# Optimization experiments

Hardware: AMD Instinct MI355X
Metric: run time of the kernel (lower is better)

Reference implementation:

```python
import jax, jax.numpy as jnp
import numpy as np

B, N = 16, 512
CFL = 0.5


def _conv(x, k):
    return jax.lax.conv_general_dilated(x, k, (1, 1), 'VALID', dimension_numbers=('NHWC', 'HWIO', 'NHWC'))


def _pad(x, p):  # p = (top, bottom, left, right) spatial pads
    return jnp.pad(x, ((0, 0), (p[0], p[1]), (p[2], p[3]), (0, 0)))


def _t(k):  # transpose(perm=[1,0,2,3]) on an HWIO kernel
    return jnp.transpose(k, (1, 0, 2, 3))


def _amper(E, Hx, Hy, beta, delta, fb, fd, fy, kf, kb, fu, fdn):
    n = N
    s1 = (_pad(beta * _conv(Hy, _t(fb)) + delta * _conv(Hy, _t(fd)) + _conv(Hy, _t(fy)), (2, 2, 2, 2))
          + _pad(_conv(Hy, _t(kf)), (2, 2, 0, n - 1))
          + _pad(_conv(Hy, _t(kb)), (2, 2, n - 1, 0))
          + _pad(_conv(Hy, _t(fu)), (2, 2, 1, n - 2))
          + _pad(_conv(Hy, _t(fdn)), (2, 2, n - 2, 1)))
    s2 = (_pad(beta * _conv(Hx, fb) + delta * _conv(Hx, fd) + _conv(Hx, fy), (2, 2, 2, 2))
          + _pad(_conv(Hx, kf), (0, n - 1, 2, 2))
          + _pad(_conv(Hx, kb), (n - 1, 0, 2, 2))
          + _pad(_conv(Hx, fu), (1, n - 2, 2, 2))
          + _pad(_conv(Hx, fdn), (n - 2, 1, 2, 2)))
    return E + CFL * (s1 - s2)


def _faraday(E, Hx, Hy, beta, delta, fb, fd, fy, kef, keb):
    n = N
    s3 = (_pad(beta * _conv(E, fb) + delta * _conv(E, fd) + _conv(E, fy), (0, 0, 1, 1))
          + _pad(_conv(E, kef), (1, 1, 0, n - 2))[:, 1:-1, :, :]
          + _pad(_conv(E, keb), (1, 1, n - 2, 0))[:, 1:-1, :, :])
    s4 = (_pad(beta * _conv(E, _t(fb)) + delta * _conv(E, _t(fd)) + _conv(E, _t(fy)), (1, 1, 0, 0))
          + _pad(_conv(E, _t(kef)), (0, n - 2, 1, 1))[:, :, 1:-1, :]
          + _pad(_conv(E, _t(keb)), (n - 2, 0, 1, 1))[:, :, 1:-1, :])
    return Hx - CFL * s3, Hy + CFL * s4


def _forward(E1, Hx1, Hy1, beta, delta, fb, fd, fy, kf, kb, fu, fdn, kef, keb):
    E2 = _amper(E1, Hx1, Hy1, beta, delta, fb, fd, fy, kf, kb, fu, fdn)
    Hx2, Hy2 = _faraday(E2, Hx1, Hy1, beta, delta, fb, fd, fy, kef, keb)
    E3 = _amper(E2, Hx2, Hy2, beta, delta, fb, fd, fy, kf, kb, fu, fdn)
    Hx3, Hy3 = _faraday(E3, Hx2, Hy2, beta, delta, fb, fd, fy, kef, keb)
    E4 = _amper(E3, Hx3, Hy3, beta, delta, fb, fd, fy, kf, kb, fu, fdn)
    Hx4, Hy4 = _faraday(E4, Hx3, Hy3, beta, delta, fb, fd, fy, kef, keb)
    return (E2, Hx2, Hy2, E3, Hx3, Hy3, E4, Hx4, Hy4)


def setup_inputs():
    key = jax.random.key(0)
    ks = jax.random.split(key, 16)
    f32 = jnp.float32
    E_shape, Hx_shape, Hy_shape = (B, N + 1, N + 1, 1), (B, N - 1, N, 1), (B, N, N - 1, 1)
    # interior 2D DRP stencils (3x4): 4-tap staggered derivative x 3-tap transverse weights
    fy = np.zeros((3, 4, 1, 1), np.float32)
    fy[1, 1, 0, 0] = -1.0
    fy[1, 2, 0, 0] = 1.0
    fb = (np.outer([1.0, -2.0, 1.0], [0.0, -1.0, 1.0, 0.0]) / 8.0).astype(np.float32).reshape(3, 4, 1, 1)
    fd = (np.outer([0.0, 1.0, 0.0], [1.0, -3.0, 3.0, -1.0]) / 24.0).astype(np.float32).reshape(3, 4, 1, 1)
    rnd = lambda k, s: 0.05 * jax.random.normal(k, s, dtype=f32)
    return {
        'E1': jax.random.normal(ks[0], E_shape, f32),
        'Hx1': jax.random.normal(ks[1], Hx_shape, f32),
        'Hy1': jax.random.normal(ks[2], Hy_shape, f32),
        'E2': jax.random.normal(ks[3], E_shape, f32),
        'Hx2': jax.random.normal(ks[4], Hx_shape, f32),
        'Hy2': jax.random.normal(ks[5], Hy_shape, f32),
        'E3': jax.random.normal(ks[6], E_shape, f32),
        'Hx3': jax.random.normal(ks[7], Hx_shape, f32),
        'Hy3': jax.random.normal(ks[8], Hy_shape, f32),
        'beta': jnp.zeros((), f32),
        'delta': jnp.asarray([0.37], f32),
        'filter_beta': jnp.asarray(fb),
        'filter_delta': jnp.asarray(fd),
        'filter_yee': jnp.asarray(fy),
        'kernel_forward': rnd(ks[9], (N - 2, 4, 1, 1)),
        'kernel_backward': rnd(ks[10], (N - 2, 4, 1, 1)),
        'fourth_up': rnd(ks[11], (N - 2, 4, 1, 1)),
        'fourth_down': rnd(ks[12], (N - 2, 4, 1, 1)),
        'kernel_e_forward': rnd(ks[13], (3, N, 1, 1)),
        'kernel_e_backward': rnd(ks[14], (3, N, 1, 1)),
    }


def reference(E1, Hx1, Hy1, E2, Hx2, Hy2, E3, Hx3, Hy3, beta, delta, filter_beta, filter_delta, filter_yee, kernel_forward, kernel_backward, fourth_up, fourth_down, kernel_e_forward, kernel_e_backward):
    # Note: the original layer unpacks E2..Hy3 but never uses them.
    return _forward(E1, Hx1, Hy1, beta, delta, filter_beta, filter_delta, filter_yee,
                    kernel_forward, kernel_backward, fourth_up, fourth_down,
                    kernel_e_forward, kernel_e_backward)
```

## Files before the change

### kernel.cpp

```cpp
#include <hip/hip_runtime.h>

#define NB 16
#define NN 512
#define NP 513
#define NM 511
#define CFLc 0.5f

#define SE (NP*NP)
#define SHX (NM*NN)
#define SHY (NN*NM)

#define NCH 8
#define OFF_A 0
#define SZ_A (NB*NCH*6*512)
#define OFF_F (OFF_A + SZ_A)
#define SZ_F (NB*NCH*4*512)
#define OFF_SE (OFF_F + SZ_F)
#define SZ_SE (NB*6*NP)
#define OFF_SH (OFF_SE + SZ_SE)
#define SZ_SH (NB*4*NM)

__device__ __forceinline__ float dot4(float4 a, float4 b) {
    return a.x*b.x + a.y*b.y + a.z*b.z + a.w*b.w;
}

__device__ __forceinline__ void ld5(const float* __restrict__ a, int mb, float4* cr) {
    const float4* a4 = (const float4*)a;
    #pragma unroll
    for (int t = 0; t < 5; t++) {
        int idx = mb - 1 + t;
        if (idx >= 0 && idx <= 509) cr[t] = a4[idx];
        else cr[t] = make_float4(0.f, 0.f, 0.f, 0.f);
    }
}

__global__ __launch_bounds__(512, 4) void k_step1(
    const float* __restrict__ E, const float* __restrict__ Hx, const float* __restrict__ Hy,
    const float* __restrict__ beta, const float* __restrict__ delta,
    const float* __restrict__ fb, const float* __restrict__ fd, const float* __restrict__ fy,
    const float* __restrict__ kf, const float* __restrict__ kb,
    const float* __restrict__ fu, const float* __restrict__ fdn,
    float* __restrict__ ws, float* __restrict__ Eout,
    float* __restrict__ Hyfix, int fix)
{
    __shared__ float s_hy[7][512];
    __shared__ float s_hx[6][512];
    __shared__ float s_strip[8][6];
    __shared__ float gsm[12];

    int bid = blockIdx.x;
    int tid = threadIdx.x;

    if (bid < 128) {
        int b = bid >> 3;
        int chunk = bid & 7;
        int j = tid;
        if (j > 508) return;
        int p0 = chunk * 64;
        int p1 = min(510, p0 + 64);
        const float* Hxb = Hx + (size_t)b*SHX;
        float akf0=0,akf1=0,akb0=0,akb1=0,afu0=0,afu1=0,afd0=0,afd1=0;
        float r0v[4], r1v[4];
        #pragma unroll
        for (int q = 0; q < 4; q++) r0v[q] = Hxb[(size_t)p0*NN + j + q];
        for (int p = p0; p < p1; p++) {
            #pragma unroll
            for (int q = 0; q < 4; q++) r1v[q] = Hxb[(size_t)(p+1)*NN + j + q];
            #pragma unroll
            for (int q = 0; q < 4; q++) {
                float ckf = kf[p*4+q], ckb = kb[p*4+q], cfu = fu[p*4+q], cfd = fdn[p*4+q];
                akf0 += r0v[q]*ckf; akf1 += r1v[q]*ckf;
                akb0 += r0v[q]*ckb; akb1 += r1v[q]*ckb;
                afu0 += r0v[q]*cfu; afu1 += r1v[q]*cfu;
                afd0 += r0v[q]*cfd; afd1 += r1v[q]*cfd;
            }
            #pragma unroll
            for (int q = 0; q < 4; q++) r0v[q] = r1v[q];
        }
        float* o = ws + OFF_A + (((size_t)b*NCH + chunk)*6)*512 + j;
        o[0*512] = akf0;
        o[1*512] = akf1 + afu0;
        o[2*512] = afu1;
        o[3*512] = afd0;
        o[4*512] = afd1 + akb0;
        o[5*512] = akb1;
        return;
    }

    if (bid >= 2192) {
        if (!fix) return;
        int b = bid - 2192;
        int c = tid;
        if (c > 510) return;
        #pragma unroll
        for (int slot = 0; slot < 4; slot++) {
            int r = (slot < 2) ? slot : 508 + slot;
            float s = 0.f;
            #pragma unroll
            for (int ch = 0; ch < NCH; ch++)
                s += ws[OFF_F + (((size_t)b*NCH + ch)*4 + slot)*512 + c];
            Hyfix[(size_t)b*SHY + (size_t)r*NM + c] =
                ws[OFF_SH + ((size_t)b*4 + slot)*NM + c] + CFLc*s;
        }
        return;
    }

    int wrk = bid - 128;
    wrk = (wrk & 7) * 258 + (wrk >> 3);
    int rg = wrk >> 4;
    int b  = wrk & 15;
    int r0 = rg * 4;

    const float* Eb  = E  + (size_t)b*SE;
    const float* Hxb = Hx + (size_t)b*SHX;
    const float* Hyb = Hy + (size_t)b*SHY;
    int c = tid;

    if (tid < 12) gsm[tid] = beta[0]*fb[tid] + delta[0]*fd[tid] + fy[tid];
    #pragma unroll
    for (int k = 0; k < 7; k++) {
        int rm = min(max(r0-2+k, 0), 511);
        int cc = min(c, 510);
        float v;
        if (fix && (rm <= 1 || rm >= 510)) {
            int slot = (rm <= 1) ? rm : rm - 508;
            float s = 0.f;
            #pragma unroll
            for (int ch = 0; ch < NCH; ch++)
                s += ws[OFF_F + (((size_t)b*NCH + ch)*4 + slot)*512 + cc];
            v = ws[OFF_SH + ((size_t)b*4 + slot)*NM + cc] + CFLc*s;
        } else {
            v = Hyb[(size_t)rm*NM + cc];
        }
        s_hy[k][c] = v;
    }
    #pragma unroll
    for (int k = 0; k < 6; k++) {
        int rm = min(max(r0-2+k, 0), 510);
        s_hx[k][c] = Hxb[(size_t)rm*NN + c];
    }
    __syncthreads();

    {
        int w = tid >> 6, lane = tid & 63;
        int jj = w >> 1;
        int ii = r0 + jj - 2;
        if (ii >= 0 && ii <= 508) {
            int h = w & 1;
            int mb = h*256 + lane*4;
            float4 hv0 = *(const float4*)&s_hy[jj+0][mb];
            float4 hv1 = *(const float4*)&s_hy[jj+1][mb];
            float4 hv2 = *(const float4*)&s_hy[jj+2][mb];
            float4 hv3 = *(const float4*)&s_hy[jj+3][mb];
            float4 hc0 = make_float4(hv0.x, hv1.x, hv2.x, hv3.x);
            float4 hc1 = make_float4(hv0.y, hv1.y, hv2.y, hv3.y);
            float4 hc2 = make_float4(hv0.z, hv1.z, hv2.z, hv3.z);
            float4 hc3 = make_float4(hv0.w, hv1.w, hv2.w, hv3.w);
            float4 cr[5];
            ld5(kf, mb, cr);
            float pkf0 = dot4(hc0,cr[1]) + dot4(hc1,cr[2]) + dot4(hc2,cr[3]) + dot4(hc3,cr[4]);
            float pkf1 = dot4(hc0,cr[0]) + dot4(hc1,cr[1]) + dot4(hc2,cr[2]) + dot4(hc3,cr[3]);
            ld5(fu, mb, cr);
            float pfu0 = dot4(hc0,cr[1]) + dot4(hc1,cr[2]) + dot4(hc2,cr[3]) + dot4(hc3,cr[4]);
            float pfu1 = dot4(hc0,cr[0]) + dot4(hc1,cr[1]) + dot4(hc2,cr[2]) + dot4(hc3,cr[3]);
            ld5(fdn, mb, cr);
            float pfd0 = dot4(hc0,cr[1]) + dot4(hc1,cr[2]) + dot4(hc2,cr[3]) + dot4(hc3,cr[4]);
            float pfd1 = dot4(hc0,cr[0]) + dot4(hc1,cr[1]) + dot4(hc2,cr[2]) + dot4(hc3,cr[3]);
            ld5(kb, mb, cr);
            float pkb0 = dot4(hc0,cr[1]) + dot4(hc1,cr[2]) + dot4(hc2,cr[3]) + dot4(hc3,cr[4]);
            float pkb1 = dot4(hc0,cr[0]) + dot4(hc1,cr[1]) + dot4(hc2,cr[2]) + dot4(hc3,cr[3]);
            float v0 = pkf0;
            float v1 = pkf1 + pfu0;
            float v2 = pfu1;
            float v3 = pfd0;
            float v4 = pfd1 + pkb0;
            float v5 = pkb1;
            #pragma unroll
            for (int off = 32; off > 0; off >>= 1) {
                v0 += __shfl_down(v0, off);
                v1 += __shfl_down(v1, off);
                v2 += __shfl_down(v2, off);
                v3 += __shfl_down(v3, off);
                v4 += __shfl_down(v4, off);
                v5 += __shfl_down(v5, off);
            }
            if (lane == 0) {
                s_strip[w][0]=v0; s_strip[w][1]=v1; s_strip[w][2]=v2;
                s_strip[w][3]=v3; s_strip[w][4]=v4; s_strip[w][5]=v5;
            }
        }
    }
    __syncthreads();

    float g[12];
    #pragma unroll
    for (int i = 0; i < 12; i++) g[i] = gsm[i];

    int cy0 = min(max(c-2,0),510), cy1 = min(max(c-1,0),510), cy2 = min(c,510);
    int cx0 = max(c-2,0), cx1 = max(c-1,0), cx3 = min(c+1,511);
    float hyv[7][3];
    #pragma unroll
    for (int k = 0; k < 7; k++) {
        hyv[k][0]=s_hy[k][cy0]; hyv[k][1]=s_hy[k][cy1]; hyv[k][2]=s_hy[k][cy2];
    }
    float hxv[6][4];
    #pragma unroll
    for (int k = 0; k < 6; k++) {
        hxv[k][0]=s_hx[k][cx0]; hxv[k][1]=s_hx[k][cx1]; hxv[k][2]=s_hx[k][c]; hxv[k][3]=s_hx[k][cx3];
    }

    bool cint = (c >= 2 && c <= 510);
    int cslot = (c==0)?0:(c==1)?1:(c==2)?2:(c==510)?3:(c==511)?4:-1;
    float* Eo = Eout + (size_t)b*SE;

    #pragma unroll
    for (int j2 = 0; j2 < 4; j2++) {
        int r = r0 + j2;
        if (r > 512) break;
        float v = Eb[(size_t)r*NP + c];
        bool rint = (r >= 2 && r <= 510);
        if (rint && cint) {
            float s1 = 0.f, s2 = 0.f;
            #pragma unroll
            for (int p = 0; p < 4; p++)
                s1 += g[p]*hyv[j2+p][0] + g[4+p]*hyv[j2+p][1] + g[8+p]*hyv[j2+p][2];
            #pragma unroll
            for (int p = 0; p < 3; p++)
                s2 += g[p*4+0]*hxv[j2+p][0] + g[p*4+1]*hxv[j2+p][1]
                    + g[p*4+2]*hxv[j2+p][2] + g[p*4+3]*hxv[j2+p][3];
            v += CFLc * (s1 - s2);
        }
        if (rint && cslot >= 0)
            v += CFLc * (s_strip[2*j2][cslot] + s_strip[2*j2+1][cslot]);
        Eo[(size_t)r*NP + c] = v;
        bool rstrip = (r <= 2 || r >= 510);
        int rslot = (r <= 2) ? r : r - 507;
        if (rstrip)
            ws[OFF_SE + ((size_t)b*6 + rslot)*NP + c] = v;
        if (c == 511) {
            float v2 = Eb[(size_t)r*NP + 512];
            if (rint) v2 += CFLc * (s_strip[2*j2][5] + s_strip[2*j2+1][5]);
            Eo[(size_t)r*NP + 512] = v2;
            if (rstrip)
                ws[OFF_SE + ((size_t)b*6 + rslot)*NP + 512] = v2;
        }
    }
}

__global__ __launch_bounds__(512, 4) void k_step2(
    const float* __restrict__ E, const float* __restrict__ Hx, const float* __restrict__ Hy,
    const float* __restrict__ beta, const float* __restrict__ delta,
    const float* __restrict__ fb, const float* __restrict__ fd, const float* __restrict__ fy,
    const float* __restrict__ kef, const float* __restrict__ keb,
    float* __restrict__ ws, float* __restrict__ Hxout, float* __restrict__ Hyout,
    float* __restrict__ Efix)
{
    __shared__ float s_e[7][520];
    __shared__ float s_fix[3][NP];
    __shared__ float s_strip2[8][4];
    __shared__ float gsm[12];

    int bid = blockIdx.x;
    int tid = threadIdx.x;

    if (bid < 128) {
        int b = bid >> 3, chunk = bid & 7;
        const float* Eb = E + (size_t)b*SE;
        bool bnd = (chunk == 0 || chunk == 7);
        int rbase = (chunk == 0) ? 0 : 510;
        if (bnd) {
            int sbase = (chunk == 0) ? 0 : 3;
            for (int t = tid; t < 3*NP; t += 512) {
                int sr = t / NP, cc = t - sr*NP;
                int slot = sbase + sr;
                float v = ws[OFF_SE + ((size_t)b*6 + slot)*NP + cc];
                if (cc >= 2 && cc <= 510) {
                    float s = 0.f;
                    #pragma unroll
                    for (int ch = 0; ch < NCH; ch++)
                        s += ws[OFF_A + (((size_t)b*NCH + ch)*6 + slot)*512 + (cc-2)];
                    v -= CFLc * s;
                }
                s_fix[sr][cc] = v;
            }
            __syncthreads();
        }
        int c = tid;
        if (c > 510) return;
        int p0 = chunk*64, p1 = p0 + 64;
        auto ldE = [&](int rr, int col) -> float {
            if (bnd) {
                unsigned d = (unsigned)(rr - rbase);
                if (d < 3u) return s_fix[d][col];
            }
            return Eb[(size_t)rr*NP + col];
        };
        float af0=0, af1=0, ab0=0, ab1=0;
        float r0v[3], r1v[3];
        #pragma unroll
        for (int q = 0; q < 3; q++) r0v[q] = ldE(p0, c + q);
        for (int p = p0; p < p1; p++) {
            #pragma unroll
            for (int q = 0; q < 3; q++) r1v[q] = ldE(p+1, c + q);
            float cf0 = kef[p], cf1 = kef[512+p], cf2 = kef[1024+p];
            float cb0 = keb[p], cb1 = keb[512+p], cb2 = keb[1024+p];
            af0 += r0v[0]*cf0 + r0v[1]*cf1 + r0v[2]*cf2;
            af1 += r1v[0]*cf0 + r1v[1]*cf1 + r1v[2]*cf2;
            ab0 += r0v[0]*cb0 + r0v[1]*cb1 + r0v[2]*cb2;
            ab1 += r1v[0]*cb0 + r1v[1]*cb1 + r1v[2]*cb2;
            r0v[0]=r1v[0]; r0v[1]=r1v[1]; r0v[2]=r1v[2];
        }
        float* o = ws + OFF_F + (((size_t)b*NCH + chunk)*4)*512 + c;
        o[0*512] = af0; o[1*512] = af1; o[2*512] = ab0; o[3*512] = ab1;
        return;
    }

    if (bid >= 2176) {
        int b = bid - 2176;
        int c = tid;
        if (c < 2 || c > 510) return;
        #pragma unroll
        for (int slot = 0; slot < 6; slot++) {
            int r = (slot < 3) ? slot : 507 + slot;
            float s = 0.f;
            #pragma unroll
            for (int ch = 0; ch < NCH; ch++)
                s += ws[OFF_A + (((size_t)b*NCH + ch)*6 + slot)*512 + (c-2)];
            Efix[(size_t)b*SE + (size_t)r*NP + c] =
                ws[OFF_SE + ((size_t)b*6 + slot)*NP + c] - CFLc*s;
        }
        return;
    }

    if (tid < 12) gsm[tid] = beta[0]*fb[tid] + delta[0]*fd[tid] + fy[tid];
    int wrk = bid - 128;
    wrk = (wrk & 7)*256 + (wrk >> 3);
    int y = wrk >> 4, b = wrk & 15;
    int r0 = y*4;
    const float* Eb = E + (size_t)b*SE;
    int c = tid;

    #pragma unroll
    for (int k = 0; k < 7; k++) {
        int rm = min(max(r0-1+k, 0), 512);
        bool strip = (rm <= 2 || rm >= 510);
        int slot = (rm <= 2) ? rm : rm - 507;
        float v;
        if (strip) {
            v = ws[OFF_SE + ((size_t)b*6 + slot)*NP + c];
            if (c >= 2 && c <= 510) {
                float s = 0.f;
                #pragma unroll
                for (int ch = 0; ch < NCH; ch++)
                    s += ws[OFF_A + (((size_t)b*NCH + ch)*6 + slot)*512 + (c-2)];
                v -= CFLc * s;
            }
        } else {
            v = Eb[(size_t)rm*NP + c];
        }
        s_e[k][c] = v;
        if (c == 511) {
            float v2 = strip ? ws[OFF_SE + ((size_t)b*6 + slot)*NP + 512]
                             : Eb[(size_t)rm*NP + 512];
            s_e[k][512] = v2;
        }
    }
    __syncthreads();

    {
        int w = tid >> 6, lane = tid & 63;
        int jj = w >> 1, h = w & 1;
        int rr = r0 + jj;
        if (rr <= 510) {
            int mb = h*256 + lane*4;
            int q4 = mb >> 2;
            float4 e0 = *(const float4*)&s_e[jj+1][mb];
            float4 e1 = *(const float4*)&s_e[jj+2][mb];
            float4 e2 = *(const float4*)&s_e[jj+3][mb];
            const float4* kef4 = (const float4*)kef;
            const float4* keb4 = (const float4*)keb;
            float4 f0 = kef4[q4], f1 = kef4[128+q4], f2 = kef4[256+q4];
            float4 b0 = keb4[q4], b1 = keb4[128+q4], b2 = keb4[256+q4];
            float af0 = dot4(e0,f0) + dot4(e1,f1) + dot4(e2,f2);
            float ab0 = dot4(e0,b0) + dot4(e1,b1) + dot4(e2,b2);
            float pw0 = (mb >= 1) ? kef[mb-1]      : 0.f;
            float pw1 = (mb >= 1) ? kef[512+mb-1]  : 0.f;
            float pw2 = (mb >= 1) ? kef[1024+mb-1] : 0.f;
            float af1 = dot4(e0, make_float4(pw0, f0.x, f0.y, f0.z))
                      + dot4(e1, make_float4(pw1, f1.x, f1.y, f1.z))
                      + dot4(e2, make_float4(pw2, f2.x, f2.y, f2.z));
            pw0 = (mb >= 1) ? keb[mb-1]      : 0.f;
            pw1 = (mb >= 1) ? keb[512+mb-1]  : 0.f;
            pw2 = (mb >= 1) ? keb[1024+mb-1] : 0.f;
            float ab1 = dot4(e0, make_float4(pw0, b0.x, b0.y, b0.z))
                      + dot4(e1, make_float4(pw1, b1.x, b1.y, b1.z))
                      + dot4(e2, make_float4(pw2, b2.x, b2.y, b2.z));
            if (mb == 508) {
                float e512_0 = s_e[jj+1][512];
                float e512_1 = s_e[jj+2][512];
                float e512_2 = s_e[jj+3][512];
                af1 += e512_0*kef[511] + e512_1*kef[1023] + e512_2*kef[1535];
                ab1 += e512_0*keb[511] + e512_1*keb[1023] + e512_2*keb[1535];
            }
            #pragma unroll
            for (int off = 32; off > 0; off >>= 1) {
                af0 += __shfl_down(af0, off);
                af1 += __shfl_down(af1, off);
                ab0 += __shfl_down(ab0, off);
                ab1 += __shfl_down(ab1, off);
            }
            if (lane == 0) {
                s_strip2[w][0]=af0; s_strip2[w][1]=af1;
                s_strip2[w][2]=ab0; s_strip2[w][3]=ab1;
            }
        }
    }
    __syncthreads();

    {
        float g[12];
        #pragma unroll
        for (int i = 0; i < 12; i++) g[i] = gsm[i];
        int c0 = max(c-1,0), c2i = min(c+1,512), c3i = min(c+2,512);
        float ev[6][4];
        #pragma unroll
        for (int k = 0; k < 6; k++) {
            ev[k][0]=s_e[k+1][c0]; ev[k][1]=s_e[k+1][c];
            ev[k][2]=s_e[k+1][c2i]; ev[k][3]=s_e[k+1][c3i];
        }
        bool cint = (c >= 1 && c <= 510);
        int slot = (c==0)?0:(c==1)?1:(c==510)?2:(c==511)?3:-1;
        const float* Hxb = Hx + (size_t)b*SHX;
        float* Ho = Hxout + (size_t)b*SHX;
        #pragma unroll
        for (int j2 = 0; j2 < 4; j2++) {
            int r = r0 + j2;
            if (r > 510) break;
            float v = Hxb[(size_t)r*NN + c];
            if (cint) {
                float s = 0.f;
                #pragma unroll
                for (int p = 0; p < 3; p++)
                    s += g[p*4+0]*ev[j2+p][0] + g[p*4+1]*ev[j2+p][1]
                       + g[p*4+2]*ev[j2+p][2] + g[p*4+3]*ev[j2+p][3];
                v -= CFLc * s;
            }
            if (slot >= 0)
                v -= CFLc * (s_strip2[2*j2][slot] + s_strip2[2*j2+1][slot]);
            Ho[(size_t)r*NN + c] = v;
        }
    }

    if (c <= 510) {
        float g[12];
        #pragma unroll
        for (int i = 0; i < 12; i++) g[i] = gsm[i];
        float ev[7][3];
        #pragma unroll
        for (int k = 0; k < 7; k++) {
            ev[k][0]=s_e[k][c]; ev[k][1]=s_e[k][c+1]; ev[k][2]=s_e[k][c+2];
        }
        const float* Hyb = Hy + (size_t)b*SHY;
        float* Ho = Hyout + (size_t)b*SHY;
        #pragma unroll
        for (int j2 = 0; j2 < 4; j2++) {
            int r = r0 + j2;
            float v = Hyb[(size_t)r*NM + c];
            if (r >= 1 && r <= 510) {
                float s = 0.f;
                #pragma unroll
                for (int p = 0; p < 4; p++)
                    s += g[p]*ev[j2+p][0] + g[4+p]*ev[j2+p][1] + g[8+p]*ev[j2+p][2];
                v += CFLc * s;
            }
            Ho[(size_t)r*NM + c] = v;
            if (r <= 1 || r >= 510)
                ws[OFF_SH + ((size_t)b*4 + ((r<=1)?r:r-508))*NM + c] = v;
        }
    }
}

__global__ __launch_bounds__(512) void k_fix_hy_final(
    const float* __restrict__ ws, float* __restrict__ Hyout)
{
    int b = blockIdx.x;
    int c = threadIdx.x;
    if (c > 510) return;
    #pragma unroll
    for (int slot = 0; slot < 4; slot++) {
        int r = (slot < 2) ? slot : 508 + slot;
        float s = 0.f;
        #pragma unroll
        for (int ch = 0; ch < NCH; ch++)
            s += ws[OFF_F + (((size_t)b*NCH + ch)*4 + slot)*512 + c];
        Hyout[(size_t)b*SHY + (size_t)r*NM + c] =
            ws[OFF_SH + ((size_t)b*4 + slot)*NM + c] + CFLc*s;
    }
}


static void run_step(const float* Ein, const float* Hxin, const float* Hyin,
                     float* Eout, float* Hxout, float* Hyout, float* ws,
                     const float* beta, const float* delta,
                     const float* fb, const float* fd, const float* fy,
                     const float* kf, const float* kb, const float* fu, const float* fdn,
                     const float* kef, const float* keb,
                     float* HyfixTarget, int fix, hipStream_t stream)
{
    dim3 blk(512);
    k_step1<<<dim3(2208), blk, 0, stream>>>(Ein, Hxin, Hyin, beta, delta,
        fb, fd, fy, kf, kb, fu, fdn, ws, Eout, HyfixTarget, fix);
    k_step2<<<dim3(2192), blk, 0, stream>>>(Eout, Hxin, Hyin, beta, delta,
        fb, fd, fy, kef, keb, ws, Hxout, Hyout, Eout);
}

extern "C" void kernel_launch(void* const* d_in, const int* in_sizes, int n_in,
                              void* d_out, int out_size, void* d_ws, size_t ws_size,
                              hipStream_t stream)
{
    const float* E1   = (const float*)d_in[0];
    const float* Hx1  = (const float*)d_in[1];
    const float* Hy1  = (const float*)d_in[2];
    const float* beta = (const float*)d_in[9];
    const float* delta= (const float*)d_in[10];
    const float* fb   = (const float*)d_in[11];
    const float* fd   = (const float*)d_in[12];
    const float* fy   = (const float*)d_in[13];
    const float* kf   = (const float*)d_in[14];
    const float* kb   = (const float*)d_in[15];
    const float* fu   = (const float*)d_in[16];
    const float* fdn  = (const float*)d_in[17];
    const float* kef  = (const float*)d_in[18];
    const float* keb  = (const float*)d_in[19];

    float* out = (float*)d_out;
    float* ws  = (float*)d_ws;
    size_t SEa = (size_t)NB * SE;
    size_t SHa = (size_t)NB * SHX;
    float* E2  = out;
    float* Hx2 = E2  + SEa;
    float* Hy2 = Hx2 + SHa;
    float* E3  = Hy2 + SHa;
    float* Hx3 = E3  + SEa;
    float* Hy3 = Hx3 + SHa;
    float* E4  = Hy3 + SHa;
    float* Hx4 = E4  + SEa;
    float* Hy4 = Hx4 + SHa;

    run_step(E1, Hx1, Hy1, E2, Hx2, Hy2, ws, beta, delta, fb, fd, fy,
             kf, kb, fu, fdn, kef, keb, nullptr, 0, stream);
    run_step(E2, Hx2, Hy2, E3, Hx3, Hy3, ws, beta, delta, fb, fd, fy,
             kf, kb, fu, fdn, kef, keb, Hy2, 1, stream);
    run_step(E3, Hx3, Hy3, E4, Hx4, Hy4, ws, beta, delta, fb, fd, fy,
             kf, kb, fu, fdn, kef, keb, Hy3, 1, stream);
    k_fix_hy_final<<<dim3(16), dim3(512), 0, stream>>>(ws, Hy4);
}
```

Before: 502.3 us.

## Fuse all step kernels into one persistent cooperative kernel with grid syncs

Result: slower. 1.370 ms (+172.7%).

```diff
diff --git a/kernel.cpp b/kernel.cpp
--- a/kernel.cpp
+++ b/kernel.cpp
@@ -1,4 +1,6 @@
 #include <hip/hip_runtime.h>
+#include <hip/hip_cooperative_groups.h>
+namespace cg = cooperative_groups;
 
 #define NB 16
 #define NN 512
@@ -20,6 +22,8 @@
 #define OFF_SH (OFF_SE + SZ_SE)
 #define SZ_SH (NB*4*NM)
 
+#define SMEM_FLOATS 6704
+
 __device__ __forceinline__ float dot4(float4 a, float4 b) {
     return a.x*b.x + a.y*b.y + a.z*b.z + a.w*b.w;
 }
@@ -34,73 +38,72 @@
     }
 }
 
-__global__ __launch_bounds__(512, 4) void k_step1(
+__device__ __forceinline__ void phaseA_tile(
+    int bid, int tid,
     const float* __restrict__ E, const float* __restrict__ Hx, const float* __restrict__ Hy,
-    const float* __restrict__ beta, const float* __restrict__ delta,
-    const float* __restrict__ fb, const float* __restrict__ fd, const float* __restrict__ fy,
     const float* __restrict__ kf, const float* __restrict__ kb,
     const float* __restrict__ fu, const float* __restrict__ fdn,
     float* __restrict__ ws, float* __restrict__ Eout,
-    float* __restrict__ Hyfix, int fix)
-{
-    __shared__ float s_hy[7][512];
-    __shared__ float s_hx[6][512];
-    __shared__ float s_strip[8][6];
-    __shared__ float gsm[12];
-
-    int bid = blockIdx.x;
-    int tid = threadIdx.x;
+    float* __restrict__ Hyfix, int fix,
+    float* __restrict__ smem, const float* __restrict__ gsm)
+{
+    float* s_hy    = smem;
+    float* s_hx    = smem + 3584;
+    float* s_strip = smem + 6656;
 
     if (bid < 128) {
         int b = bid >> 3;
         int chunk = bid & 7;
         int j = tid;
-        if (j > 508) return;
-        int p0 = chunk * 64;
-        int p1 = min(510, p0 + 64);
-        const float* Hxb = Hx + (size_t)b*SHX;
-        float akf0=0,akf1=0,akb0=0,akb1=0,afu0=0,afu1=0,afd0=0,afd1=0;
-        float r0v[4], r1v[4];
-        #pragma unroll
-        for (int q = 0; q < 4; q++) r0v[q] = Hxb[(size_t)p0*NN + j + q];
-        for (int p = p0; p < p1; p++) {
-            #pragma unroll
-            for (int q = 0; q < 4; q++) r1v[q] = Hxb[(size_t)(p+1)*NN + j + q];
-            #pragma unroll
-            for (int q = 0; q < 4; q++) {
-                float ckf = kf[p*4+q], ckb = kb[p*4+q], cfu = fu[p*4+q], cfd = fdn[p*4+q];
-                akf0 += r0v[q]*ckf; akf1 += r1v[q]*ckf;
-                akb0 += r0v[q]*ckb; akb1 += r1v[q]*ckb;
-                afu0 += r0v[q]*cfu; afu1 += r1v[q]*cfu;
-                afd0 += r0v[q]*cfd; afd1 += r1v[q]*cfd;
-            }
-            #pragma unroll
-            for (int q = 0; q < 4; q++) r0v[q] = r1v[q];
-        }
-        float* o = ws + OFF_A + (((size_t)b*NCH + chunk)*6)*512 + j;
-        o[0*512] = akf0;
-        o[1*512] = akf1 + afu0;
-        o[2*512] = afu1;
-        o[3*512] = afd0;
-        o[4*512] = afd1 + akb0;
-        o[5*512] = akb1;
+        if (j <= 508) {
+            int p0 = chunk * 64;
+            int p1 = min(510, p0 + 64);
+            const float* Hxb = Hx + (size_t)b*SHX;
+            float akf0=0,akf1=0,akb0=0,akb1=0,afu0=0,afu1=0,afd0=0,afd1=0;
+            float r0v[4], r1v[4];
+            #pragma unroll
+            for (int q = 0; q < 4; q++) r0v[q] = Hxb[(size_t)p0*NN + j + q];
+            for (int p = p0; p < p1; p++) {
+                #pragma unroll
+                for (int q = 0; q < 4; q++) r1v[q] = Hxb[(size_t)(p+1)*NN + j + q];
+                #pragma unroll
+                for (int q = 0; q < 4; q++) {
+                    float ckf = kf[p*4+q], ckb = kb[p*4+q], cfu = fu[p*4+q], cfd = fdn[p*4+q];
+                    akf0 += r0v[q]*ckf; akf1 += r1v[q]*ckf;
+                    akb0 += r0v[q]*ckb; akb1 += r1v[q]*ckb;
+                    afu0 += r0v[q]*cfu; afu1 += r1v[q]*cfu;
+                    afd0 += r0v[q]*cfd; afd1 += r1v[q]*cfd;
+                }
+                #pragma unroll
+                for (int q = 0; q < 4; q++) r0v[q] = r1v[q];
+            }
+            float* o = ws + OFF_A + (((size_t)b*NCH + chunk)*6)*512 + j;
+            o[0*512] = akf0;
+            o[1*512] = akf1 + afu0;
+            o[2*512] = afu1;
+            o[3*512] = afd0;
+            o[4*512] = afd1 + akb0;
+            o[5*512] = akb1;
+        }
         return;
     }
 
     if (bid >= 2192) {
-        if (!fix) return;
-        int b = bid - 2192;
-        int c = tid;
-        if (c > 510) return;
-        #pragma unroll
-        for (int slot = 0; slot < 4; slot++) {
-            int r = (slot < 2) ? slot : 508 + slot;
-            float s = 0.f;
-            #pragma unroll
-            for (int ch = 0; ch < NCH; ch++)
-                s += ws[OFF_F + (((size_t)b*NCH + ch)*4 + slot)*512 + c];
-            Hyfix[(size_t)b*SHY + (size_t)r*NM + c] =
-                ws[OFF_SH + ((size_t)b*4 + slot)*NM + c] + CFLc*s;
+        if (fix) {
+            int b = bid - 2192;
+            int c = tid;
+            if (c <= 510) {
+                #pragma unroll
+                for (int slot = 0; slot < 4; slot++) {
+                    int r = (slot < 2) ? slot : 508 + slot;
+                    float s = 0.f;
+                    #pragma unroll
+                    for (int ch = 0; ch < NCH; ch++)
+                        s += ws[OFF_F + (((size_t)b*NCH + ch)*4 + slot)*512 + c];
+                    Hyfix[(size_t)b*SHY + (size_t)r*NM + c] =
+                        ws[OFF_SH + ((size_t)b*4 + slot)*NM + c] + CFLc*s;
+                }
+            }
         }
         return;
     }
@@ -116,7 +119,6 @@
     const float* Hyb = Hy + (size_t)b*SHY;
     int c = tid;
 
-    if (tid < 12) gsm[tid] = beta[0]*fb[tid] + delta[0]*fd[tid] + fy[tid];
     #pragma unroll
     for (int k = 0; k < 7; k++) {
         int rm = min(max(r0-2+k, 0), 511);
@@ -132,12 +134,12 @@
         } else {
             v = Hyb[(size_t)rm*NM + cc];
         }
-        s_hy[k][c] = v;
+        s_hy[k*512 + c] = v;
     }
     #pragma unroll
     for (int k = 0; k < 6; k++) {
         int rm = min(max(r0-2+k, 0), 510);
-        s_hx[k][c] = Hxb[(size_t)rm*NN + c];
+        s_hx[k*512 + c] = Hxb[(size_t)rm*NN + c];
     }
     __syncthreads();
 
@@ -148,10 +150,10 @@
         if (ii >= 0 && ii <= 508) {
             int h = w & 1;
             int mb = h*256 + lane*4;
-            float4 hv0 = *(const float4*)&s_hy[jj+0][mb];
-            float4 hv1 = *(const float4*)&s_hy[jj+1][mb];
-            float4 hv2 = *(const float4*)&s_hy[jj+2][mb];
-            float4 hv3 = *(const float4*)&s_hy[jj+3][mb];
+            float4 hv0 = *(const float4*)&s_hy[(jj+0)*512 + mb];
+            float4 hv1 = *(const float4*)&s_hy[(jj+1)*512 + mb];
+            float4 hv2 = *(const float4*)&s_hy[(jj+2)*512 + mb];
+            float4 hv3 = *(const float4*)&s_hy[(jj+3)*512 + mb];
             float4 hc0 = make_float4(hv0.x, hv1.x, hv2.x, hv3.x);
             float4 hc1 = make_float4(hv0.y, hv1.y, hv2.y, hv3.y);
             float4 hc2 = make_float4(hv0.z, hv1.z, hv2.z, hv3.z);
@@ -185,8 +187,8 @@
                 v5 += __shfl_down(v5, off);
             }
             if (lane == 0) {
-                s_strip[w][0]=v0; s_strip[w][1]=v1; s_strip[w][2]=v2;
-                s_strip[w][3]=v3; s_strip[w][4]=v4; s_strip[w][5]=v5;
+                s_strip[w*6+0]=v0; s_strip[w*6+1]=v1; s_strip[w*6+2]=v2;
+                s_strip[w*6+3]=v3; s_strip[w*6+4]=v4; s_strip[w*6+5]=v5;
             }
         }
     }
@@ -201,12 +203,13 @@
     float hyv[7][3];
     #pragma unroll
     for (int k = 0; k < 7; k++) {
-        hyv[k][0]=s_hy[k][cy0]; hyv[k][1]=s_hy[k][cy1]; hyv[k][2]=s_hy[k][cy2];
+        hyv[k][0]=s_hy[k*512+cy0]; hyv[k][1]=s_hy[k*512+cy1]; hyv[k][2]=s_hy[k*512+cy2];
     }
     float hxv[6][4];
     #pragma unroll
     for (int k = 0; k < 6; k++) {
-        hxv[k][0]=s_hx[k][cx0]; hxv[k][1]=s_hx[k][cx1]; hxv[k][2]=s_hx[k][c]; hxv[k][3]=s_hx[k][cx3];
+        hxv[k][0]=s_hx[k*512+cx0]; hxv[k][1]=s_hx[k*512+cx1];
+        hxv[k][2]=s_hx[k*512+c];   hxv[k][3]=s_hx[k*512+cx3];
     }
 
     bool cint = (c >= 2 && c <= 510);
@@ -231,7 +234,7 @@
             v += CFLc * (s1 - s2);
         }
         if (rint && cslot >= 0)
-            v += CFLc * (s_strip[2*j2][cslot] + s_strip[2*j2+1][cslot]);
+            v += CFLc * (s_strip[(2*j2)*6 + cslot] + s_strip[(2*j2+1)*6 + cslot]);
         Eo[(size_t)r*NP + c] = v;
         bool rstrip = (r <= 2 || r >= 510);
         int rslot = (r <= 2) ? r : r - 507;
@@ -239,7 +242,7 @@
             ws[OFF_SE + ((size_t)b*6 + rslot)*NP + c] = v;
         if (c == 511) {
             float v2 = Eb[(size_t)r*NP + 512];
-            if (rint) v2 += CFLc * (s_strip[2*j2][5] + s_strip[2*j2+1][5]);
+            if (rint) v2 += CFLc * (s_strip[(2*j2)*6 + 5] + s_strip[(2*j2+1)*6 + 5]);
             Eo[(size_t)r*NP + 512] = v2;
             if (rstrip)
                 ws[OFF_SE + ((size_t)b*6 + rslot)*NP + 512] = v2;
@@ -247,21 +250,17 @@
     }
 }
 
-__global__ __launch_bounds__(512, 4) void k_step2(
+__device__ __forceinline__ void phaseB_tile(
+    int bid, int tid,
     const float* __restrict__ E, const float* __restrict__ Hx, const float* __restrict__ Hy,
-    const float* __restrict__ beta, const float* __restrict__ delta,
-    const float* __restrict__ fb, const float* __restrict__ fd, const float* __restrict__ fy,
     const float* __restrict__ kef, const float* __restrict__ keb,
     float* __restrict__ ws, float* __restrict__ Hxout, float* __restrict__ Hyout,
-    float* __restrict__ Efix)
-{
-    __shared__ float s_e[7][520];
-    __shared__ float s_fix[3][NP];
-    __shared__ float s_strip2[8][4];
-    __shared__ float gsm[12];
-
-    int bid = blockIdx.x;
-    int tid = threadIdx.x;
+    float* __restrict__ Efix,
+    float* __restrict__ smem, const float* __restrict__ gsm)
+{
+    float* s_e      = smem;
+    float* s_fix    = smem + 3640;
+    float* s_strip2 = smem + 5179;
 
     if (bid < 128) {
         int b = bid >> 3, chunk = bid & 7;
@@ -281,58 +280,59 @@
                         s += ws[OFF_A + (((size_t)b*NCH + ch)*6 + slot)*512 + (cc-2)];
                     v -= CFLc * s;
                 }
-                s_fix[sr][cc] = v;
+                s_fix[sr*NP + cc] = v;
             }
             __syncthreads();
         }
         int c = tid;
-        if (c > 510) return;
-        int p0 = chunk*64, p1 = p0 + 64;
-        auto ldE = [&](int rr, int col) -> float {
-            if (bnd) {
-                unsigned d = (unsigned)(rr - rbase);
-                if (d < 3u) return s_fix[d][col];
-            }
-            return Eb[(size_t)rr*NP + col];
-        };
-        float af0=0, af1=0, ab0=0, ab1=0;
-        float r0v[3], r1v[3];
-        #pragma unroll
-        for (int q = 0; q < 3; q++) r0v[q] = ldE(p0, c + q);
-        for (int p = p0; p < p1; p++) {
-            #pragma unroll
-            for (int q = 0; q < 3; q++) r1v[q] = ldE(p+1, c + q);
-            float cf0 = kef[p], cf1 = kef[512+p], cf2 = kef[1024+p];
-            float cb0 = keb[p], cb1 = keb[512+p], cb2 = keb[1024+p];
-            af0 += r0v[0]*cf0 + r0v[1]*cf1 + r0v[2]*cf2;
-            af1 += r1v[0]*cf0 + r1v[1]*cf1 + r1v[2]*cf2;
-            ab0 += r0v[0]*cb0 + r0v[1]*cb1 + r0v[2]*cb2;
-            ab1 += r1v[0]*cb0 + r1v[1]*cb1 + r1v[2]*cb2;
-            r0v[0]=r1v[0]; r0v[1]=r1v[1]; r0v[2]=r1v[2];
-        }
-        float* o = ws + OFF_F + (((size_t)b*NCH + chunk)*4)*512 + c;
-        o[0*512] = af0; o[1*512] = af1; o[2*512] = ab0; o[3*512] = ab1;
+        if (c <= 510) {
+            int p0 = chunk*64, p1 = p0 + 64;
+            auto ldE = [&](int rr, int col) -> float {
+                if (bnd) {
+                    unsigned d = (unsigned)(rr - rbase);
+                    if (d < 3u) return s_fix[d*NP + col];
+                }
+                return Eb[(size_t)rr*NP + col];
+            };
+            float af0=0, af1=0, ab0=0, ab1=0;
+            float r0v[3], r1v[3];
+            #pragma unroll
+            for (int q = 0; q < 3; q++) r0v[q] = ldE(p0, c + q);
+            for (int p = p0; p < p1; p++) {
+                #pragma unroll
+                for (int q = 0; q < 3; q++) r1v[q] = ldE(p+1, c + q);
+                float cf0 = kef[p], cf1 = kef[512+p], cf2 = kef[1024+p];
+                float cb0 = keb[p], cb1 = keb[512+p], cb2 = keb[1024+p];
+                af0 += r0v[0]*cf0 + r0v[1]*cf1 + r0v[2]*cf2;
+                af1 += r1v[0]*cf0 + r1v[1]*cf1 + r1v[2]*cf2;
+                ab0 += r0v[0]*cb0 + r0v[1]*cb1 + r0v[2]*cb2;
+                ab1 += r1v[0]*cb0 + r1v[1]*cb1 + r1v[2]*cb2;
+                r0v[0]=r1v[0]; r0v[1]=r1v[1]; r0v[2]=r1v[2];
+            }
+            float* o = ws + OFF_F + (((size_t)b*NCH + chunk)*4)*512 + c;
+            o[0*512] = af0; o[1*512] = af1; o[2*512] = ab0; o[3*512] = ab1;
+        }
         return;
     }
 
     if (bid >= 2176) {
         int b = bid - 2176;
         int c = tid;
-        if (c < 2 || c > 510) return;
-        #pragma unroll
-        for (int slot = 0; slot < 6; slot++) {
-            int r = (slot < 3) ? slot : 507 + slot;
-            float s = 0.f;
-            #pragma unroll
-            for (int ch = 0; ch < NCH; ch++)
-                s += ws[OFF_A + (((size_t)b*NCH + ch)*6 + slot)*512 + (c-2)];
-            Efix[(size_t)b*SE + (size_t)r*NP + c] =
-                ws[OFF_SE + ((size_t)b*6 + slot)*NP + c] - CFLc*s;
+        if (c >= 2 && c <= 510) {
+            #pragma unroll
+            for (int slot = 0; slot < 6; slot++) {
+                int r = (slot < 3) ? slot : 507 + slot;
+                float s = 0.f;
+                #pragma unroll
+                for (int ch = 0; ch < NCH; ch++)
+                    s += ws[OFF_A + (((size_t)b*NCH + ch)*6 + slot)*512 + (c-2)];
+                Efix[(size_t)b*SE + (size_t)r*NP + c] =
+                    ws[OFF_SE + ((size_t)b*6 + slot)*NP + c] - CFLc*s;
+            }
         }
         return;
     }
 
-    if (tid < 12) gsm[tid] = beta[0]*fb[tid] + delta[0]*fd[tid] + fy[tid];
     int wrk = bid - 128;
     wrk = (wrk & 7)*256 + (wrk >> 3);
     int y = wrk >> 4, b = wrk & 15;
@@ -358,11 +358,11 @@
         } else {
             v = Eb[(size_t)rm*NP + c];
         }
-        s_e[k][c] = v;
+        s_e[k*520 + c] = v;
         if (c == 511) {
             float v2 = strip ? ws[OFF_SE + ((size_t)b*6 + slot)*NP + 512]
                              : Eb[(size_t)rm*NP + 512];
-            s_e[k][512] = v2;
+            s_e[k*520 + 512] = v2;
         }
     }
     __syncthreads();
@@ -374,9 +374,9 @@
         if (rr <= 510) {
             int mb = h*256 + lane*4;
             int q4 = mb >> 2;
-            float4 e0 = *(const float4*)&s_e[jj+1][mb];
-            float4 e1 = *(const float4*)&s_e[jj+2][mb];
-            float4 e2 = *(const float4*)&s_e[jj+3][mb];
+            float4 e0 = *(const float4*)&s_e[(jj+1)*520 + mb];
+            float4 e1 = *(const float4*)&s_e[(jj+2)*520 + mb];
+            float4 e2 = *(const float4*)&s_e[(jj+3)*520 + mb];
             const float4* kef4 = (const float4*)kef;
             const float4* keb4 = (const float4*)keb;
             float4 f0 = kef4[q4], f1 = kef4[128+q4], f2 = kef4[256+q4];
@@ -396,9 +396,9 @@
                       + dot4(e1, make_float4(pw1, b1.x, b1.y, b1.z))
                       + dot4(e2, make_float4(pw2, b2.x, b2.y, b2.z));
             if (mb == 508) {
-                float e512_0 = s_e[jj+1][512];
-                float e512_1 = s_e[jj+2][512];
-                float e512_2 = s_e[jj+3][512];
+                float e512_0 = s_e[(jj+1)*520 + 512];
+                float e512_1 = s_e[(jj+2)*520 + 512];
+                float e512_2 = s_e[(jj+3)*520 + 512];
                 af1 += e512_0*kef[511] + e512_1*kef[1023] + e512_2*kef[1535];
                 ab1 += e512_0*keb[511] + e512_1*keb[1023] + e512_2*keb[1535];
             }
@@ -410,8 +410,8 @@
                 ab1 += __shfl_down(ab1, off);
             }
             if (lane == 0) {
-                s_strip2[w][0]=af0; s_strip2[w][1]=af1;
-                s_strip2[w][2]=ab0; s_strip2[w][3]=ab1;
+                s_strip2[w*4+0]=af0; s_strip2[w*4+1]=af1;
+                s_strip2[w*4+2]=ab0; s_strip2[w*4+3]=ab1;
             }
         }
     }
@@ -425,8 +425,8 @@
         float ev[6][4];
         #pragma unroll
         for (int k = 0; k < 6; k++) {
-            ev[k][0]=s_e[k+1][c0]; ev[k][1]=s_e[k+1][c];
-            ev[k][2]=s_e[k+1][c2i]; ev[k][3]=s_e[k+1][c3i];
+            ev[k][0]=s_e[(k+1)*520+c0]; ev[k][1]=s_e[(k+1)*520+c];
+            ev[k][2]=s_e[(k+1)*520+c2i]; ev[k][3]=s_e[(k+1)*520+c3i];
         }
         bool cint = (c >= 1 && c <= 510);
         int slot = (c==0)?0:(c==1)?1:(c==510)?2:(c==511)?3:-1;
@@ -446,7 +446,7 @@
                 v -= CFLc * s;
             }
             if (slot >= 0)
-                v -= CFLc * (s_strip2[2*j2][slot] + s_strip2[2*j2+1][slot]);
+                v -= CFLc * (s_strip2[(2*j2)*4 + slot] + s_strip2[(2*j2+1)*4 + slot]);
             Ho[(size_t)r*NN + c] = v;
         }
     }
@@ -458,7 +458,7 @@
         float ev[7][3];
         #pragma unroll
         for (int k = 0; k < 7; k++) {
-            ev[k][0]=s_e[k][c]; ev[k][1]=s_e[k][c+1]; ev[k][2]=s_e[k][c+2];
+            ev[k][0]=s_e[k*520+c]; ev[k][1]=s_e[k*520+c+1]; ev[k][2]=s_e[k*520+c+2];
         }
         const float* Hyb = Hy + (size_t)b*SHY;
         float* Ho = Hyout + (size_t)b*SHY;
@@ -480,39 +480,124 @@
     }
 }
 
-__global__ __launch_bounds__(512) void k_fix_hy_final(
+__device__ __forceinline__ void final_tile(int bid, int tid,
     const float* __restrict__ ws, float* __restrict__ Hyout)
 {
-    int b = blockIdx.x;
-    int c = threadIdx.x;
-    if (c > 510) return;
-    #pragma unroll
-    for (int slot = 0; slot < 4; slot++) {
-        int r = (slot < 2) ? slot : 508 + slot;
-        float s = 0.f;
+    int b = bid;
+    int c = tid;
+    if (c <= 510) {
         #pragma unroll
-        for (int ch = 0; ch < NCH; ch++)
-            s += ws[OFF_F + (((size_t)b*NCH + ch)*4 + slot)*512 + c];
-        Hyout[(size_t)b*SHY + (size_t)r*NM + c] =
-            ws[OFF_SH + ((size_t)b*4 + slot)*NM + c] + CFLc*s;
-    }
-}
-
-
-static void run_step(const float* Ein, const float* Hxin, const float* Hyin,
-                     float* Eout, float* Hxout, float* Hyout, float* ws,
-                     const float* beta, const float* delta,
-                     const float* fb, const float* fd, const float* fy,
-                     const float* kf, const float* kb, const float* fu, const float* fdn,
-                     const float* kef, const float* keb,
-                     float* HyfixTarget, int fix, hipStream_t stream)
-{
-    dim3 blk(512);
-    k_step1<<<dim3(2208), blk, 0, stream>>>(Ein, Hxin, Hyin, beta, delta,
-        fb, fd, fy, kf, kb, fu, fdn, ws, Eout, HyfixTarget, fix);
-    k_step2<<<dim3(2192), blk, 0, stream>>>(Eout, Hxin, Hyin, beta, delta,
-        fb, fd, fy, kef, keb, ws, Hxout, Hyout, Eout);
-}
+        for (int slot = 0; slot < 4; slot++) {
+            int r = (slot < 2) ? slot : 508 + slot;
+            float s = 0.f;
+            #pragma unroll
+            for (int ch = 0; ch < NCH; ch++)
+                s += ws[OFF_F + (((size_t)b*NCH + ch)*4 + slot)*512 + c];
+            Hyout[(size_t)b*SHY + (size_t)r*NM + c] =
+                ws[OFF_SH + ((size_t)b*4 + slot)*NM + c] + CFLc*s;
+        }
+    }
+}
+
+__global__ __launch_bounds__(512, 4) void k_mega(
+    const float* E1, const float* Hx1, const float* Hy1,
+    const float* beta, const float* delta,
+    const float* fb, const float* fd, const float* fy,
+    const float* kf, const float* kb, const float* fu, const float* fdn,
+    const float* kef, const float* keb,
+    float* ws, float* out)
+{
+    __shared__ __align__(16) float smem[SMEM_FLOATS];
+    __shared__ float gsm[12];
+    int tid = threadIdx.x;
+    if (tid < 12) gsm[tid] = beta[0]*fb[tid] + delta[0]*fd[tid] + fy[tid];
+    __syncthreads();
+
+    cg::grid_group grid = cg::this_grid();
+
+    size_t SEa = (size_t)NB * SE;
+    size_t SHa = (size_t)NB * SHX;
+    float* E2  = out;
+    float* Hx2 = E2  + SEa;
+    float* Hy2 = Hx2 + SHa;
+    float* E3  = Hy2 + SHa;
+    float* Hx3 = E3  + SEa;
+    float* Hy3 = Hx3 + SHa;
+    float* E4  = Hy3 + SHa;
+    float* Hx4 = E4  + SEa;
+    float* Hy4 = Hx4 + SHa;
+
+    float* Eo[3]  = {E2, E3, E4};
+    float* Hxo[3] = {Hx2, Hx3, Hx4};
+    float* Hyo[3] = {Hy2, Hy3, Hy4};
+
+    #pragma unroll 1
+    for (int s = 0; s < 3; s++) {
+        const float* Ecur  = (s==0) ? E1  : Eo[s-1];
+        const float* Hxcur = (s==0) ? Hx1 : Hxo[s-1];
+        const float* Hycur = (s==0) ? Hy1 : Hyo[s-1];
+        int fix = (s > 0) ? 1 : 0;
+        float* Hyfix = fix ? Hyo[s-1] : nullptr;
+
+        for (int t = blockIdx.x; t < 2208; t += gridDim.x) {
+            __syncthreads();
+            phaseA_tile(t, tid, Ecur, Hxcur, Hycur, kf, kb, fu, fdn,
+                        ws, Eo[s], Hyfix, fix, smem, gsm);
+        }
+        __threadfence();
+        grid.sync();
+
+        for (int t = blockIdx.x; t < 2192; t += gridDim.x) {
+            __syncthreads();
+            phaseB_tile(t, tid, Eo[s], Hxcur, Hycur, kef, keb,
+                        ws, Hxo[s], Hyo[s], Eo[s], smem, gsm);
+        }
+        __threadfence();
+        grid.sync();
+    }
+
+    for (int t = blockIdx.x; t < 16; t += gridDim.x)
+        final_tile(t, tid, ws, Hyo[2]);
+}
+
+__global__ __launch_bounds__(512, 4) void k_stepA(
+    const float* __restrict__ E, const float* __restrict__ Hx, const float* __restrict__ Hy,
+    const float* __restrict__ beta, const float* __restrict__ delta,
+    const float* __restrict__ fb, const float* __restrict__ fd, const float* __restrict__ fy,
+    const float* __restrict__ kf, const float* __restrict__ kb,
+    const float* __restrict__ fu, const float* __restrict__ fdn,
+    float* __restrict__ ws, float* __restrict__ Eout,
+    float* __restrict__ Hyfix, int fix)
+{
+    __shared__ __align__(16) float smem[SMEM_FLOATS];
+    __shared__ float gsm[12];
+    int tid = threadIdx.x;
+    if (tid < 12) gsm[tid] = beta[0]*fb[tid] + delta[0]*fd[tid] + fy[tid];
+    __syncthreads();
+    phaseA_tile(blockIdx.x, tid, E, Hx, Hy, kf, kb, fu, fdn, ws, Eout, Hyfix, fix, smem, gsm);
+}
+
+__global__ __launch_bounds__(512, 4) void k_stepB(
+    const float* __restrict__ E, const float* __restrict__ Hx, const float* __restrict__ Hy,
+    const float* __restrict__ beta, const float* __restrict__ delta,
+    const float* __restrict__ fb, const float* __restrict__ fd, const float* __restrict__ fy,
+    const float* __restrict__ kef, const float* __restrict__ keb,
+    float* __restrict__ ws, float* __restrict__ Hxout, float* __restrict__ Hyout,
+    float* __restrict__ Efix)
+{
+    __shared__ __align__(16) float smem[SMEM_FLOATS];
+    __shared__ float gsm[12];
+    int tid = threadIdx.x;
+    if (tid < 12) gsm[tid] = beta[0]*fb[tid] + delta[0]*fd[tid] + fy[tid];
+    __syncthreads();
+    phaseB_tile(blockIdx.x, tid, E, Hx, Hy, kef, keb, ws, Hxout, Hyout, Efix, smem, gsm);
+}
+
+__global__ __launch_bounds__(512) void k_final(const float* __restrict__ ws, float* __restrict__ Hyout)
+{
+    final_tile(blockIdx.x, threadIdx.x, ws, Hyout);
+}
+
 
 extern "C" void kernel_launch(void* const* d_in, const int* in_sizes, int n_in,
                               void* d_out, int out_size, void* d_ws, size_t ws_size,
@@ -535,23 +620,66 @@
 
     float* out = (float*)d_out;
     float* ws  = (float*)d_ws;
-    size_t SEa = (size_t)NB * SE;
-    size_t SHa = (size_t)NB * SHX;
-    float* E2  = out;
-    float* Hx2 = E2  + SEa;
-    float* Hy2 = Hx2 + SHa;
-    float* E3  = Hy2 + SHa;
-    float* Hx3 = E3  + SEa;
-    float* Hy3 = Hx3 + SHa;
-    float* E4  = Hy3 + SHa;
-    float* Hx4 = E4  + SEa;
-    float* Hy4 = Hx4 + SHa;
-
-    run_step(E1, Hx1, Hy1, E2, Hx2, Hy2, ws, beta, delta, fb, fd, fy,
-             kf, kb, fu, fdn, kef, keb, nullptr, 0, stream);
-    run_step(E2, Hx2, Hy2, E3, Hx3, Hy3, ws, beta, delta, fb, fd, fy,
-             kf, kb, fu, fdn, kef, keb, Hy2, 1, stream);
-    run_step(E3, Hx3, Hy3, E4, Hx4, Hy4, ws, beta, delta, fb, fd, fy,
-             kf, kb, fu, fdn, kef, keb, Hy3, 1, stream);
-    k_fix_hy_final<<<dim3(16), dim3(512), 0, stream>>>(ws, Hy4);
-}
+
+    static int s_grid = -2;
+    if (s_grid == -2) {
+        int nb = 0;
+        hipError_t e = hipOccupancyMaxActiveBlocksPerMultiprocessor(&nb, k_mega, 512, 0);
+        if (e == hipSuccess && nb > 0) {
+            hipDeviceProp_t prop;
+            int dev = 0;
+            hipGetDevice(&dev);
+            if (hipGetDeviceProperties(&prop, dev) == hipSuccess && prop.multiProcessorCount > 0) {
+                long g = (long)nb * prop.multiProcessorCount;
+                s_grid = (int)(g > 2208 ? 2208 : g);
+            } else s_grid = 0;
+        } else s_grid = 0;
+    }
+
+    bool launched = false;
+    if (s_grid > 0) {
+        const float *aE1=E1, *aHx1=Hx1, *aHy1=Hy1, *aBeta=beta, *aDelta=delta;
+        const float *aFb=fb, *aFd=fd, *aFy=fy, *aKf=kf, *aKb=kb, *aFu=fu, *aFdn=fdn;
+        const float *aKef=kef, *aKeb=keb;
+        float *aWs=ws, *aOut=out;
+        void* args[16] = {
+            (void*)&aE1, (void*)&aHx1, (void*)&aHy1, (void*)&aBeta, (void*)&aDelta,
+            (void*)&aFb, (void*)&aFd, (void*)&aFy, (void*)&aKf, (void*)&aKb,
+            (void*)&aFu, (void*)&aFdn, (void*)&aKef, (void*)&aKeb,
+            (void*)&aWs, (void*)&aOut
+        };
+        hipError_t e = hipLaunchCooperativeKernel(k_mega, dim3(s_grid), dim3(512),
+                                                  args, 0, stream);
+        launched = (e == hipSuccess);
+        if (!launched) s_grid = 0;
+    }
+
+    if (!launched) {
+        size_t SEa = (size_t)NB * SE;
+        size_t SHa = (size_t)NB * SHX;
+        float* E2  = out;
+        float* Hx2 = E2  + SEa;
+        float* Hy2 = Hx2 + SHa;
+        float* E3  = Hy2 + SHa;
+        float* Hx3 = E3  + SEa;
+        float* Hy3 = Hx3 + SHa;
+        float* E4  = Hy3 + SHa;
+        float* Hx4 = E4  + SEa;
+        float* Hy4 = Hx4 + SHa;
+        dim3 blk(512);
+
+        k_stepA<<<dim3(2208), blk, 0, stream>>>(E1, Hx1, Hy1, beta, delta, fb, fd, fy,
+            kf, kb, fu, fdn, ws, E2, nullptr, 0);
+        k_stepB<<<dim3(2192), blk, 0, stream>>>(E2, Hx1, Hy1, beta, delta, fb, fd, fy,
+            kef, keb, ws, Hx2, Hy2, E2);
+        k_stepA<<<dim3(2208), blk, 0, stream>>>(E2, Hx2, Hy2, beta, delta, fb, fd, fy,
+            kf, kb, fu, fdn, ws, E3, Hy2, 1);
+        k_stepB<<<dim3(2192), blk, 0, stream>>>(E3, Hx2, Hy2, beta, delta, fb, fd, fy,
+            kef, keb, ws, Hx3, Hy3, E3);
+        k_stepA<<<dim3(2208), blk, 0, stream>>>(E3, Hx3, Hy3, beta, delta, fb, fd, fy,
+            kf, kb, fu, fdn, ws, E4, Hy3, 1);
+        k_stepB<<<dim3(2192), blk, 0, stream>>>(E4, Hx3, Hy3, beta, delta, fb, fd, fy,
+            kef, keb, ws, Hx4, Hy4, E4);
+        k_final<<<dim3(16), blk, 0, stream>>>(ws, Hy4);
+    }
+}
```
